# Optimization experiments

Measured on AMD Instinct MI355X. Metric: run time of the kernel, lower is better.

The kernel has to match this reference:

```python
import jax, jax.numpy as jnp
import numpy as np

N = 100000
E = 800000
D = 128
THETA = (0.5, 0.3, 0.2)
NEG_SLOPE = 0.01  # torch F.leaky_relu default


def setup_inputs() -> dict:
    key = jax.random.key(0)
    ks = jax.random.split(key, 16)
    inv = 1.0 / np.sqrt(D)
    return {
        "src": jax.random.randint(ks[0], (E,), 0, N),
        "dst": jax.random.randint(ks[1], (E,), 0, N),
        "x0": jax.random.normal(ks[2], (N, D), jnp.float32),
        "x": jax.random.normal(ks[3], (N, D), jnp.float32),
        "e": jax.random.normal(ks[4], (N, D), jnp.float32),
        "labels": jax.random.randint(ks[5], (N,), 0, 2),
        "nid": jax.random.randint(ks[6], (N // 2,), 0, N),
        "alpha": jnp.full((1,), 0.5, jnp.float32),
        "emb": jax.random.normal(ks[7], (3, D), jnp.float32).at[2].set(0.0),  # padding_idx=2
        "pred_w1": jax.random.normal(ks[8], (D, D), jnp.float32) * inv,
        "pred_b1": jnp.zeros((D,), jnp.float32),
        "pred_w2": jax.random.normal(ks[9], (2, D), jnp.float32) * inv,
        "pred_b2": jnp.zeros((2,), jnp.float32),
        "weights": jax.random.uniform(ks[10], (2 * D, D), jnp.float32, -inv, inv),
        "lin_w": jax.random.normal(ks[11], (D, 2 * D), jnp.float32) * inv,
        "lin_b": jnp.zeros((D,), jnp.float32),
    }


def reference(src, dst, x0, x, e, labels, nid, alpha, emb,
              pred_w1, pred_b1, pred_w2, pred_b2, weights, lin_w, lin_b):
    # Predictor: MLP -> 2 logits, prob of class 1
    h = jax.nn.relu(x @ pred_w1.T + pred_b1)
    logits = h @ pred_w2.T + pred_b2                     # [N, 2]
    prob = jax.nn.softmax(logits, axis=1)[:, 1]          # [N]

    # NodeLabelEmbedding: soft mix of rows 0 and 1
    x_node = (1.0 - prob)[:, None] * emb[0] + prob[:, None] * emb[1]
    x_ = x
    xk = x + alpha * x_node

    # degree norm from edge list (in-degrees at dst)
    degs = jax.ops.segment_sum(jnp.ones_like(dst, dtype=xk.dtype), dst, num_segments=N)
    dinv = jnp.clip(degs, 1.0, None) ** -0.5             # [N]
    dinv = dinv[:, None]

    def unn_laplacian(feat):
        # feat - D^-1/2 A D^-1/2 feat  (messages src -> dst)
        msg = jax.ops.segment_sum((feat * dinv)[src], dst, num_segments=N)
        return feat - msg * dinv

    hi = THETA[0] * xk
    for k in range(1, len(THETA)):
        xk = unn_laplacian(xk)
        hi = hi + THETA[k] * xk

    hi = jnp.concatenate([hi, x_], axis=1)               # [N, 2D]
    outputs = hi @ weights                               # [N, D]
    out = jnp.concatenate([e, outputs], axis=1)          # [N, 2D]
    out = jax.nn.leaky_relu(out @ lin_w.T + lin_b, NEG_SLOPE)
    return out + x0                                      # residual
```

## Files before the change

kernel.cpp:

```cpp
#include <hip/hip_runtime.h>

#define N_NODES 100000
#define N_EDGES 800000
#define D 128

#define G_MLP 1563
#define G_DEG 3125
#define G_PRE 192

typedef __attribute__((ext_vector_type(8))) short short8;
typedef __attribute__((ext_vector_type(4))) float f32x4;

__device__ inline unsigned short f2bf(float f) {
  unsigned u = __float_as_uint(f);
  unsigned r = (u + 0x7fffu + ((u >> 16) & 1u)) >> 16;
  return (unsigned short)r;
}
__device__ inline void bfma8(float* acc, const uint4 v, float d) {
  acc[0] = fmaf(__uint_as_float(v.x << 16), d, acc[0]);
  acc[1] = fmaf(__uint_as_float(v.x & 0xffff0000u), d, acc[1]);
  acc[2] = fmaf(__uint_as_float(v.y << 16), d, acc[2]);
  acc[3] = fmaf(__uint_as_float(v.y & 0xffff0000u), d, acc[3]);
  acc[4] = fmaf(__uint_as_float(v.z << 16), d, acc[4]);
  acc[5] = fmaf(__uint_as_float(v.z & 0xffff0000u), d, acc[5]);
  acc[6] = fmaf(__uint_as_float(v.w << 16), d, acc[6]);
  acc[7] = fmaf(__uint_as_float(v.w & 0xffff0000u), d, acc[7]);
}
__device__ inline void unpack8(float* o, const uint4 v) {
  o[0] = __uint_as_float(v.x << 16); o[1] = __uint_as_float(v.x & 0xffff0000u);
  o[2] = __uint_as_float(v.y << 16); o[3] = __uint_as_float(v.y & 0xffff0000u);
  o[4] = __uint_as_float(v.z << 16); o[5] = __uint_as_float(v.z & 0xffff0000u);
  o[6] = __uint_as_float(v.w << 16); o[7] = __uint_as_float(v.w & 0xffff0000u);
}
__device__ inline uint4 pack8(const float* v) {
  uint4 r;
  r.x = (unsigned)f2bf(v[0]) | ((unsigned)f2bf(v[1]) << 16);
  r.y = (unsigned)f2bf(v[2]) | ((unsigned)f2bf(v[3]) << 16);
  r.z = (unsigned)f2bf(v[4]) | ((unsigned)f2bf(v[5]) << 16);
  r.w = (unsigned)f2bf(v[6]) | ((unsigned)f2bf(v[7]) << 16);
  return r;
}

__global__ __launch_bounds__(256, 4)
void k_front(const float* __restrict__ x, const float* __restrict__ w1,
             const float* __restrict__ w2, const float* __restrict__ b1,
             const float* __restrict__ b2, const float* __restrict__ emb,
             const float* __restrict__ alpha_p, unsigned short* __restrict__ xk_bf,
             const int* __restrict__ dst, int* __restrict__ degs,
             const float* __restrict__ weights, const float* __restrict__ lin_w,
             unsigned short* __restrict__ wbt) {
  int tid = threadIdx.x;
  int bid = blockIdx.x;

  if (bid >= G_MLP) {
    if (bid < G_MLP + G_DEG) {
      int e = (bid - G_MLP) * 256 + tid;
      if (e < N_EDGES) atomicAdd(&degs[dst[e]], 1);
    } else {
      int gid = (bid - G_MLP - G_DEG) * 256 + tid;
      int k = gid >> 7, d = gid & 127;
      float v;
      if (k < 128) {
        v = lin_w[d * 256 + k];
      } else {
        const float* wrow = weights + (k - 128) * 128;
        const float* lcol = lin_w + d * 256 + 128;
        float s = 0.f;
        for (int j = 0; j < 128; j++) s += wrow[j] * lcol[j];
        v = s;
      }
      wbt[d * 392 + k] = f2bf(v);
    }
    return;
  }

  __shared__ __align__(16) float xsT[32 * 68];
  __shared__ __align__(16) float w1sT[32 * 128];
  __shared__ float zbuf[64];
  __shared__ float pbuf[64];

  int lane = tid & 63;
  int wave = tid >> 6;
  int n0 = bid * 64;

  int d8 = tid & 15;
  int n4 = tid >> 4;
  float acc[4][8];
  #pragma unroll
  for (int a = 0; a < 4; a++)
    #pragma unroll
    for (int c = 0; c < 8; c++) acc[a][c] = 0.f;

  for (int p = 0; p < 4; p++) {
    __syncthreads();
    {
      int j = tid >> 1;
      int kg0 = (tid & 1) * 4;
      const float4* wr = (const float4*)(w1 + j * 128 + p * 32);
      #pragma unroll
      for (int c = 0; c < 4; c++) {
        float4 v = wr[kg0 + c];
        int k = (kg0 + c) * 4;
        w1sT[(k + 0) * 128 + j] = v.x;
        w1sT[(k + 1) * 128 + j] = v.y;
        w1sT[(k + 2) * 128 + j] = v.z;
        w1sT[(k + 3) * 128 + j] = v.w;
      }
    }
    {
      int n = lane;
      int gn = n0 + n;
      int k8 = wave * 8;
      const float4* xr = (const float4*)(x + (size_t)gn * 128 + p * 32 + k8);
      float4 v0 = make_float4(0.f, 0.f, 0.f, 0.f), v1 = v0;
      if (gn < N_NODES) { v0 = xr[0]; v1 = xr[1]; }
      xsT[(k8 + 0) * 68 + n] = v0.x;
      xsT[(k8 + 1) * 68 + n] = v0.y;
      xsT[(k8 + 2) * 68 + n] = v0.z;
      xsT[(k8 + 3) * 68 + n] = v0.w;
      xsT[(k8 + 4) * 68 + n] = v1.x;
      xsT[(k8 + 5) * 68 + n] = v1.y;
      xsT[(k8 + 6) * 68 + n] = v1.z;
      xsT[(k8 + 7) * 68 + n] = v1.w;
    }
    __syncthreads();

    for (int kk = 0; kk < 32; kk += 4) {
      float wq[4][8];
      float4 f[4];
      #pragma unroll
      for (int q = 0; q < 4; q++) {
        const float4* wr = (const float4*)(w1sT + (kk + q) * 128 + d8 * 8);
        float4 a = wr[0], b = wr[1];
        wq[q][0] = a.x; wq[q][1] = a.y; wq[q][2] = a.z; wq[q][3] = a.w;
        wq[q][4] = b.x; wq[q][5] = b.y; wq[q][6] = b.z; wq[q][7] = b.w;
        f[q] = *(const float4*)(xsT + (kk + q) * 68 + n4 * 4);
      }
      #pragma unroll
      for (int q = 0; q < 4; q++) {
        #pragma unroll
        for (int c = 0; c < 8; c++) {
          acc[0][c] += f[q].x * wq[q][c];
          acc[1][c] += f[q].y * wq[q][c];
          acc[2][c] += f[q].z * wq[q][c];
          acc[3][c] += f[q].w * wq[q][c];
        }
      }
    }
  }

  {
    int j0 = d8 * 8;
    float bb[8], wd[8];
    #pragma unroll
    for (int c = 0; c < 8; c++) {
      bb[c] = b1[j0 + c];
      wd[c] = w2[128 + j0 + c] - w2[j0 + c];
    }
    #pragma unroll
    for (int a = 0; a < 4; a++) {
      float s = 0.f;
      #pragma unroll
      for (int c = 0; c < 8; c++) {
        float h = fmaxf(acc[a][c] + bb[c], 0.f);
        s += h * wd[c];
      }
      s += __shfl_down(s, 8);
      s += __shfl_down(s, 4);
      s += __shfl_down(s, 2);
      s += __shfl_down(s, 1);
      if (d8 == 0) zbuf[n4 * 4 + a] = s;
    }
  }
  __syncthreads();
  if (tid < 64) {
    float db2 = b2[1] - b2[0];
    float z = zbuf[tid] + db2;
    pbuf[tid] = 1.f / (1.f + expf(-z));
  }
  __syncthreads();

  {
    float al = alpha_p[0];
    int d4 = tid & 31;
    const float4 e0 = ((const float4*)emb)[d4];
    const float4 e1 = ((const float4*)(emb + 128))[d4];
    #pragma unroll
    for (int i = 0; i < 8; i++) {
      int n = i * 8 + (tid >> 5);
      int gn = n0 + n;
      if (gn >= N_NODES) continue;
      float p = pbuf[n];
      float c0 = al * (1.f - p), c1 = al * p;
      float4 xv = ((const float4*)x)[(size_t)gn * 32 + d4];
      float o0 = xv.x + c0 * e0.x + c1 * e1.x;
      float o1 = xv.y + c0 * e0.y + c1 * e1.y;
      float o2 = xv.z + c0 * e0.z + c1 * e1.z;
      float o3 = xv.w + c0 * e0.w + c1 * e1.w;
      ushort4 ov = make_ushort4(f2bf(o0), f2bf(o1), f2bf(o2), f2bf(o3));
      ((ushort4*)xk_bf)[(size_t)gn * 32 + d4] = ov;
    }
  }
}

__global__ void k_scan1(const int* __restrict__ degs, int* __restrict__ offs,
                        int* __restrict__ aux) {
  __shared__ int s[256];
  int tid = threadIdx.x;
  int i = blockIdx.x * 256 + tid;
  int v = (i < N_NODES) ? degs[i] : 0;
  int sum = v;
  s[tid] = sum; __syncthreads();
  for (int off = 1; off < 256; off <<= 1) {
    int t = (tid >= off) ? s[tid - off] : 0;
    __syncthreads();
    sum += t; s[tid] = sum;
    __syncthreads();
  }
  if (i < N_NODES) offs[i] = sum - v;
  if (tid == 255) aux[blockIdx.x] = sum;
}

__global__ void k_scan2(const int* __restrict__ aux, int* __restrict__ aux2, int nblk) {
  __shared__ int s[512];
  int tid = threadIdx.x;
  int v = (tid < nblk) ? aux[tid] : 0;
  int sum = v;
  s[tid] = sum; __syncthreads();
  for (int off = 1; off < 512; off <<= 1) {
    int t = (tid >= off) ? s[tid - off] : 0;
    __syncthreads();
    sum += t; s[tid] = sum;
    __syncthreads();
  }
  aux2[tid] = sum - v;
}

__global__ void k_scan3(int* __restrict__ offs, const int* __restrict__ aux2,
                        const int* __restrict__ degs, float* __restrict__ dinv) {
  int i = blockIdx.x * 256 + threadIdx.x;
  if (i < N_NODES) {
    offs[i] += aux2[blockIdx.x];
    dinv[i] = rsqrtf(fmaxf((float)degs[i], 1.0f));
  }
}

__global__ void k_fill(const int* __restrict__ src, const int* __restrict__ dst,
                       const int* __restrict__ offs, int* __restrict__ cursor,
                       int* __restrict__ csr) {
  int e = blockIdx.x * 256 + threadIdx.x;
  if (e < N_EDGES) {
    int d = dst[e];
    int pos = offs[d] + atomicAdd(&cursor[d], 1);
    csr[pos] = src[e];
  }
}

template <int PASS>
__global__ __launch_bounds__(256)
void k_gather(const unsigned short* __restrict__ feat,
              unsigned short* __restrict__ feat_out,
              float* __restrict__ hi,
              unsigned short* __restrict__ ahi,
              const int* __restrict__ csr, const int* __restrict__ offs,
              const int* __restrict__ degs, const float* __restrict__ dinv) {
  int node = blockIdx.x * 4 + (threadIdx.x >> 6);
  int lane = threadIdx.x & 63;
  int quad = lane >> 4;
  int l16 = lane & 15;
  int start = offs[node];
  int cnt = degs[node];
  const uint4* f16 = (const uint4*)feat;
  float acc[8];
  #pragma unroll
  for (int i = 0; i < 8; i++) acc[i] = 0.f;

  int j = 0;
  for (; j + 8 <= cnt; j += 8) {
    int sa = csr[start + j + quad];
    int sb = csr[start + j + 4 + quad];
    float da = dinv[sa], db = dinv[sb];
    uint4 va = f16[(size_t)sa * 16 + l16];
    uint4 vb = f16[(size_t)sb * 16 + l16];
    bfma8(acc, va, da);
    bfma8(acc, vb, db);
  }
  if (j + 4 <= cnt) {
    int s = csr[start + j + quad];
    float d = dinv[s];
    uint4 v = f16[(size_t)s * 16 + l16];
    bfma8(acc, v, d);
    j += 4;
  }
  int rem = cnt - j;
  if (quad < rem) {
    int s = csr[start + j + quad];
    float d = dinv[s];
    uint4 v = f16[(size_t)s * 16 + l16];
    bfma8(acc, v, d);
  }

  #pragma unroll
  for (int i = 0; i < 8; i++) {
    acc[i] += __shfl_down(acc[i], 32);
    acc[i] += __shfl_down(acc[i], 16);
  }

  if (quad == 0) {
    float dvi = dinv[node];
    float old[8], nw[8];
    unpack8(old, f16[(size_t)node * 16 + l16]);
    #pragma unroll
    for (int i = 0; i < 8; i++) nw[i] = old[i] - acc[i] * dvi;
    if (PASS == 1) {
      ((uint4*)feat_out)[(size_t)node * 16 + l16] = pack8(nw);
      float h[8];
      #pragma unroll
      for (int i = 0; i < 8; i++) h[i] = 0.5f * old[i] + 0.3f * nw[i];
      float4* hp = (float4*)(hi + (size_t)node * 128 + l16 * 8);
      hp[0] = make_float4(h[0], h[1], h[2], h[3]);
      hp[1] = make_float4(h[4], h[5], h[6], h[7]);
    } else {
      const float4* hp = (const float4*)(hi + (size_t)node * 128 + l16 * 8);
      float4 a = hp[0], b = hp[1];
      float h[8] = {a.x, a.y, a.z, a.w, b.x, b.y, b.z, b.w};
      #pragma unroll
      for (int i = 0; i < 8; i++) h[i] += 0.2f * nw[i];
      ((uint4*)ahi)[(size_t)node * 16 + l16] = pack8(h);
    }
  }
}

__global__ __launch_bounds__(256)
__attribute__((amdgpu_waves_per_eu(4, 4)))
void k_gemm2(const float* __restrict__ ein, const unsigned short* __restrict__ ahi,
             const float* __restrict__ x, const unsigned short* __restrict__ wbt,
             const float* __restrict__ lin_b, const float* __restrict__ x0,
             float* __restrict__ out) {
  __shared__ __align__(16) unsigned short Bs[32 * 392];
  int tid = threadIdx.x;
  int lane = tid & 63, wv = tid >> 6;
  int quad = lane >> 4, l16 = lane & 15;
  int n0 = blockIdx.x * 64;
  int rA = n0 + wv * 16 + l16;
  if (rA >= N_NODES) rA = N_NODES - 1;
  int kq = quad * 8;

  short8 af[12];
  #pragma unroll
  for (int kb = 0; kb < 4; kb++) {
    const float4* p = (const float4*)(ein + (size_t)rA * 128 + kb * 32 + kq);
    float4 a = p[0], b = p[1];
    short8 t;
    t[0] = (short)f2bf(a.x); t[1] = (short)f2bf(a.y);
    t[2] = (short)f2bf(a.z); t[3] = (short)f2bf(a.w);
    t[4] = (short)f2bf(b.x); t[5] = (short)f2bf(b.y);
    t[6] = (short)f2bf(b.z); t[7] = (short)f2bf(b.w);
    af[kb] = t;
  }
  #pragma unroll
  for (int kb = 0; kb < 4; kb++)
    af[4 + kb] = *(const short8*)(ahi + (size_t)rA * 128 + kb * 32 + kq);
  #pragma unroll
  for (int kb = 0; kb < 4; kb++) {
    const float4* p = (const float4*)(x + (size_t)rA * 128 + kb * 32 + kq);
    float4 a = p[0], b = p[1];
    short8 t;
    t[0] = (short)f2bf(a.x); t[1] = (short)f2bf(a.y);
    t[2] = (short)f2bf(a.z); t[3] = (short)f2bf(a.w);
    t[4] = (short)f2bf(b.x); t[5] = (short)f2bf(b.y);
    t[6] = (short)f2bf(b.z); t[7] = (short)f2bf(b.w);
    af[8 + kb] = t;
  }

  f32x4 acc[8];
  #pragma unroll
  for (int i = 0; i < 8; i++) acc[i] = (f32x4){0.f, 0.f, 0.f, 0.f};

  #pragma unroll
  for (int ch = 0; ch < 4; ch++) {
    if (ch) __syncthreads();
    {
      const uint4* W = (const uint4*)wbt;
      uint4* B4 = (uint4*)Bs;
      int r = tid >> 3, c0 = tid & 7;
      #pragma unroll
      for (int i = 0; i < 7; i++) {
        int c = c0 + i * 8;
        if (c < 49) B4[r * 49 + c] = W[(ch * 32 + r) * 49 + c];
      }
    }
    __syncthreads();
    #pragma unroll
    for (int kb = 0; kb < 12; kb++) {
      short8 a = af[kb];
      #pragma unroll
      for (int t = 0; t < 2; t++) {
        short8 b = *(const short8*)(Bs + (t * 16 + l16) * 392 + kb * 32 + kq);
        acc[ch * 2 + t] = __builtin_amdgcn_mfma_f32_16x16x32_bf16(a, b, acc[ch * 2 + t], 0, 0, 0);
      }
    }
  }

  #pragma unroll
  for (int idx = 0; idx < 8; idx++) {
    int col = (idx >> 1) * 32 + (idx & 1) * 16 + l16;
    float bl = lin_b[col];
    #pragma unroll
    for (int r = 0; r < 4; r++) {
      int gn = n0 + wv * 16 + quad * 4 + r;
      if (gn < N_NODES) {
        float v = acc[idx][r] + bl;
        v = (v > 0.f) ? v : 0.01f * v;
        out[(size_t)gn * 128 + col] = v + x0[(size_t)gn * 128 + col];
      }
    }
  }
}

extern "C" void kernel_launch(void* const* d_in, const int* in_sizes, int n_in,
                              void* d_out, int out_size, void* d_ws, size_t ws_size,
                              hipStream_t stream) {
  const int*   src     = (const int*)d_in[0];
  const int*   dst     = (const int*)d_in[1];
  const float* x0      = (const float*)d_in[2];
  const float* x       = (const float*)d_in[3];
  const float* ein     = (const float*)d_in[4];
  const float* alpha   = (const float*)d_in[7];
  const float* emb     = (const float*)d_in[8];
  const float* w1      = (const float*)d_in[9];
  const float* b1      = (const float*)d_in[10];
  const float* w2      = (const float*)d_in[11];
  const float* b2      = (const float*)d_in[12];
  const float* weights = (const float*)d_in[13];
  const float* lin_w   = (const float*)d_in[14];
  const float* lin_b   = (const float*)d_in[15];
  float* out = (float*)d_out;

  unsigned short* xk_bf  = (unsigned short*)d_ws;
  unsigned short* xk1_bf = xk_bf  + (size_t)N_NODES * 128;
  unsigned short* ahi    = xk1_bf + (size_t)N_NODES * 128;
  unsigned short* wbt    = ahi    + (size_t)N_NODES * 128;
  float* dinv = (float*)(wbt + 128 * 392);
  int* degs   = (int*)(dinv + N_NODES);
  int* offs   = degs + N_NODES;
  int* cursor = offs + N_NODES;
  int* aux    = cursor + N_NODES;
  int* aux2   = aux + 512;
  int* csr    = aux2 + 512;

  hipMemsetAsync(degs, 0, sizeof(int) * 3 * (size_t)N_NODES, stream);

  int gN = (N_NODES + 255) / 256;
  int gE = (N_EDGES + 255) / 256;

  k_front<<<G_MLP + G_DEG + G_PRE, 256, 0, stream>>>(
      x, w1, w2, b1, b2, emb, alpha, xk_bf, dst, degs, weights, lin_w, wbt);

  k_scan1<<<gN, 256, 0, stream>>>(degs, offs, aux);
  k_scan2<<<1, 512, 0, stream>>>(aux, aux2, gN);
  k_scan3<<<gN, 256, 0, stream>>>(offs, aux2, degs, dinv);
  k_fill <<<gE, 256, 0, stream>>>(src, dst, offs, cursor, csr);

  float* hi = out;
  k_gather<1><<<N_NODES / 4, 256, 0, stream>>>(xk_bf,  xk1_bf, hi, nullptr, csr, offs, degs, dinv);
  k_gather<2><<<N_NODES / 4, 256, 0, stream>>>(xk1_bf, nullptr, hi, ahi,    csr, offs, degs, dinv);

  k_gemm2<<<(N_NODES + 63) / 64, 256, 0, stream>>>(ein, ahi, x, wbt, lin_b, x0, out);
}
```

Baseline: 449.5 us.

## Read GEMM2 weight fragments directly from global memory instead of LDS staging

The final GEMM kernel no longer stages the combined weight matrix into shared memory in four chunks with barriers. Each lane now loads its B fragments straight from global (cache-resident) weights, and A fragments are converted per k-step inside the loop rather than all held in registers up front. This removes LDS traffic, barriers and the occupancy cap, trading them for many more global/L1 loads of the small weight matrix per wave.

```diff
diff --git a/kernel.cpp b/kernel.cpp
--- a/kernel.cpp
+++ b/kernel.cpp
@@ -332,12 +332,10 @@
 }
 
 __global__ __launch_bounds__(256)
-__attribute__((amdgpu_waves_per_eu(4, 4)))
 void k_gemm2(const float* __restrict__ ein, const unsigned short* __restrict__ ahi,
              const float* __restrict__ x, const unsigned short* __restrict__ wbt,
              const float* __restrict__ lin_b, const float* __restrict__ x0,
              float* __restrict__ out) {
-  __shared__ __align__(16) unsigned short Bs[32 * 392];
   int tid = threadIdx.x;
   int lane = tid & 63, wv = tid >> 6;
   int quad = lane >> 4, l16 = lane & 15;
@@ -346,71 +344,48 @@
   if (rA >= N_NODES) rA = N_NODES - 1;
   int kq = quad * 8;
 
-  short8 af[12];
-  #pragma unroll
-  for (int kb = 0; kb < 4; kb++) {
-    const float4* p = (const float4*)(ein + (size_t)rA * 128 + kb * 32 + kq);
-    float4 a = p[0], b = p[1];
-    short8 t;
-    t[0] = (short)f2bf(a.x); t[1] = (short)f2bf(a.y);
-    t[2] = (short)f2bf(a.z); t[3] = (short)f2bf(a.w);
-    t[4] = (short)f2bf(b.x); t[5] = (short)f2bf(b.y);
-    t[6] = (short)f2bf(b.z); t[7] = (short)f2bf(b.w);
-    af[kb] = t;
-  }
-  #pragma unroll
-  for (int kb = 0; kb < 4; kb++)
-    af[4 + kb] = *(const short8*)(ahi + (size_t)rA * 128 + kb * 32 + kq);
-  #pragma unroll
-  for (int kb = 0; kb < 4; kb++) {
-    const float4* p = (const float4*)(x + (size_t)rA * 128 + kb * 32 + kq);
-    float4 a = p[0], b = p[1];
-    short8 t;
-    t[0] = (short)f2bf(a.x); t[1] = (short)f2bf(a.y);
-    t[2] = (short)f2bf(a.z); t[3] = (short)f2bf(a.w);
-    t[4] = (short)f2bf(b.x); t[5] = (short)f2bf(b.y);
-    t[6] = (short)f2bf(b.z); t[7] = (short)f2bf(b.w);
-    af[8 + kb] = t;
-  }
-
   f32x4 acc[8];
   #pragma unroll
   for (int i = 0; i < 8; i++) acc[i] = (f32x4){0.f, 0.f, 0.f, 0.f};
 
-  #pragma unroll
-  for (int ch = 0; ch < 4; ch++) {
-    if (ch) __syncthreads();
-    {
-      const uint4* W = (const uint4*)wbt;
-      uint4* B4 = (uint4*)Bs;
-      int r = tid >> 3, c0 = tid & 7;
-      #pragma unroll
-      for (int i = 0; i < 7; i++) {
-        int c = c0 + i * 8;
-        if (c < 49) B4[r * 49 + c] = W[(ch * 32 + r) * 49 + c];
-      }
-    }
-    __syncthreads();
-    #pragma unroll
-    for (int kb = 0; kb < 12; kb++) {
-      short8 a = af[kb];
-      #pragma unroll
-      for (int t = 0; t < 2; t++) {
-        short8 b = *(const short8*)(Bs + (t * 16 + l16) * 392 + kb * 32 + kq);
-        acc[ch * 2 + t] = __builtin_amdgcn_mfma_f32_16x16x32_bf16(a, b, acc[ch * 2 + t], 0, 0, 0);
-      }
-    }
-  }
-
-  #pragma unroll
-  for (int idx = 0; idx < 8; idx++) {
-    int col = (idx >> 1) * 32 + (idx & 1) * 16 + l16;
+  const unsigned short* bp = wbt + (size_t)l16 * 392 + kq;
+
+  #pragma unroll
+  for (int kb = 0; kb < 12; kb++) {
+    short8 a;
+    if (kb < 4) {
+      const float4* p = (const float4*)(ein + (size_t)rA * 128 + kb * 32 + kq);
+      float4 u = p[0], v = p[1];
+      a[0] = (short)f2bf(u.x); a[1] = (short)f2bf(u.y);
+      a[2] = (short)f2bf(u.z); a[3] = (short)f2bf(u.w);
+      a[4] = (short)f2bf(v.x); a[5] = (short)f2bf(v.y);
+      a[6] = (short)f2bf(v.z); a[7] = (short)f2bf(v.w);
+    } else if (kb < 8) {
+      a = *(const short8*)(ahi + (size_t)rA * 128 + (kb - 4) * 32 + kq);
+    } else {
+      const float4* p = (const float4*)(x + (size_t)rA * 128 + (kb - 8) * 32 + kq);
+      float4 u = p[0], v = p[1];
+      a[0] = (short)f2bf(u.x); a[1] = (short)f2bf(u.y);
+      a[2] = (short)f2bf(u.z); a[3] = (short)f2bf(u.w);
+      a[4] = (short)f2bf(v.x); a[5] = (short)f2bf(v.y);
+      a[6] = (short)f2bf(v.z); a[7] = (short)f2bf(v.w);
+    }
+    #pragma unroll
+    for (int ct = 0; ct < 8; ct++) {
+      short8 b = *(const short8*)(bp + (size_t)ct * 16 * 392 + kb * 32);
+      acc[ct] = __builtin_amdgcn_mfma_f32_16x16x32_bf16(a, b, acc[ct], 0, 0, 0);
+    }
+  }
+
+  #pragma unroll
+  for (int ct = 0; ct < 8; ct++) {
+    int col = ct * 16 + l16;
     float bl = lin_b[col];
     #pragma unroll
     for (int r = 0; r < 4; r++) {
       int gn = n0 + wv * 16 + quad * 4 + r;
       if (gn < N_NODES) {
-        float v = acc[idx][r] + bl;
+        float v = acc[ct][r] + bl;
         v = (v > 0.f) ? v : 0.01f * v;
         out[(size_t)gn * 128 + col] = v + x0[(size_t)gn * 128 + col];
       }
```

Result: slower. 490.4 us (+9.1%).

## Pre-swizzle GEMM weights into MFMA fragment order and double-buffer LDS loads

Applied to the files above, without the earlier changes.

The weight-prep stage now stores the combined bf16 weight matrix already laid out in the MFMA B-fragment order, so each lane reads one contiguous 16-byte vector from LDS. The final GEMM kernel double-buffers the weight chunks, prefetching the next chunk into registers while the MFMAs for the current chunk run, which removes one barrier per chunk. The fixed waves-per-EU attribute is also dropped. LDS use grows to two 24 KB buffers, which may lower occupancy.

```diff
diff --git a/kernel.cpp b/kernel.cpp
--- a/kernel.cpp
+++ b/kernel.cpp
@@ -48,7 +48,7 @@
              const float* __restrict__ alpha_p, unsigned short* __restrict__ xk_bf,
              const int* __restrict__ dst, int* __restrict__ degs,
              const float* __restrict__ weights, const float* __restrict__ lin_w,
-             unsigned short* __restrict__ wbt) {
+             unsigned short* __restrict__ wfr) {
   int tid = threadIdx.x;
   int bid = blockIdx.x;
 
@@ -69,7 +69,10 @@
         for (int j = 0; j < 128; j++) s += wrow[j] * lcol[j];
         v = s;
       }
-      wbt[d * 392 + k] = f2bf(v);
+      int ct = d >> 4, kb = k >> 5;
+      int lane = (((k >> 3) & 3) << 4) | (d & 15);
+      int j = k & 7;
+      wfr[((ct * 12 + kb) << 9) + (lane << 3) + j] = f2bf(v);
     }
     return;
   }
@@ -332,12 +335,11 @@
 }
 
 __global__ __launch_bounds__(256)
-__attribute__((amdgpu_waves_per_eu(4, 4)))
 void k_gemm2(const float* __restrict__ ein, const unsigned short* __restrict__ ahi,
-             const float* __restrict__ x, const unsigned short* __restrict__ wbt,
+             const float* __restrict__ x, const unsigned short* __restrict__ wfr,
              const float* __restrict__ lin_b, const float* __restrict__ x0,
              float* __restrict__ out) {
-  __shared__ __align__(16) unsigned short Bs[32 * 392];
+  __shared__ __align__(16) unsigned short Bs[2][24 * 512];
   int tid = threadIdx.x;
   int lane = tid & 63, wv = tid >> 6;
   int quad = lane >> 4, l16 = lane & 15;
@@ -377,40 +379,53 @@
   #pragma unroll
   for (int i = 0; i < 8; i++) acc[i] = (f32x4){0.f, 0.f, 0.f, 0.f};
 
+  const uint4* W4 = (const uint4*)wfr;
+
+  {
+    uint4 tmp[6];
+    #pragma unroll
+    for (int i = 0; i < 6; i++) tmp[i] = W4[tid + i * 256];
+    uint4* B4 = (uint4*)Bs[0];
+    #pragma unroll
+    for (int i = 0; i < 6; i++) B4[tid + i * 256] = tmp[i];
+  }
+  __syncthreads();
+
   #pragma unroll
   for (int ch = 0; ch < 4; ch++) {
-    if (ch) __syncthreads();
-    {
-      const uint4* W = (const uint4*)wbt;
-      uint4* B4 = (uint4*)Bs;
-      int r = tid >> 3, c0 = tid & 7;
-      #pragma unroll
-      for (int i = 0; i < 7; i++) {
-        int c = c0 + i * 8;
-        if (c < 49) B4[r * 49 + c] = W[(ch * 32 + r) * 49 + c];
-      }
-    }
-    __syncthreads();
-    #pragma unroll
-    for (int kb = 0; kb < 12; kb++) {
-      short8 a = af[kb];
-      #pragma unroll
-      for (int t = 0; t < 2; t++) {
-        short8 b = *(const short8*)(Bs + (t * 16 + l16) * 392 + kb * 32 + kq);
-        acc[ch * 2 + t] = __builtin_amdgcn_mfma_f32_16x16x32_bf16(a, b, acc[ch * 2 + t], 0, 0, 0);
-      }
-    }
-  }
-
-  #pragma unroll
-  for (int idx = 0; idx < 8; idx++) {
-    int col = (idx >> 1) * 32 + (idx & 1) * 16 + l16;
+    int cur = ch & 1;
+    uint4 tmp[6];
+    if (ch < 3) {
+      #pragma unroll
+      for (int i = 0; i < 6; i++) tmp[i] = W4[(ch + 1) * 1536 + tid + i * 256];
+    }
+    const unsigned short* Bc = Bs[cur];
+    #pragma unroll
+    for (int ctl = 0; ctl < 2; ctl++) {
+      #pragma unroll
+      for (int kb = 0; kb < 12; kb++) {
+        short8 b = *(const short8*)(Bc + (ctl * 12 + kb) * 512 + (lane << 3));
+        acc[ch * 2 + ctl] =
+            __builtin_amdgcn_mfma_f32_16x16x32_bf16(af[kb], b, acc[ch * 2 + ctl], 0, 0, 0);
+      }
+    }
+    if (ch < 3) {
+      uint4* B4 = (uint4*)Bs[cur ^ 1];
+      #pragma unroll
+      for (int i = 0; i < 6; i++) B4[tid + i * 256] = tmp[i];
+      __syncthreads();
+    }
+  }
+
+  #pragma unroll
+  for (int ct = 0; ct < 8; ct++) {
+    int col = ct * 16 + l16;
     float bl = lin_b[col];
     #pragma unroll
     for (int r = 0; r < 4; r++) {
       int gn = n0 + wv * 16 + quad * 4 + r;
       if (gn < N_NODES) {
-        float v = acc[idx][r] + bl;
+        float v = acc[ct][r] + bl;
         v = (v > 0.f) ? v : 0.01f * v;
         out[(size_t)gn * 128 + col] = v + x0[(size_t)gn * 128 + col];
       }
@@ -440,8 +455,8 @@
   unsigned short* xk_bf  = (unsigned short*)d_ws;
   unsigned short* xk1_bf = xk_bf  + (size_t)N_NODES * 128;
   unsigned short* ahi    = xk1_bf + (size_t)N_NODES * 128;
-  unsigned short* wbt    = ahi    + (size_t)N_NODES * 128;
-  float* dinv = (float*)(wbt + 128 * 392);
+  unsigned short* wfr    = ahi    + (size_t)N_NODES * 128;
+  float* dinv = (float*)(wfr + 128 * 392);
   int* degs   = (int*)(dinv + N_NODES);
   int* offs   = degs + N_NODES;
   int* cursor = offs + N_NODES;
@@ -455,7 +470,7 @@
   int gE = (N_EDGES + 255) / 256;
 
   k_front<<<G_MLP + G_DEG + G_PRE, 256, 0, stream>>>(
-      x, w1, w2, b1, b2, emb, alpha, xk_bf, dst, degs, weights, lin_w, wbt);
+      x, w1, w2, b1, b2, emb, alpha, xk_bf, dst, degs, weights, lin_w, wfr);
 
   k_scan1<<<gN, 256, 0, stream>>>(degs, offs, aux);
   k_scan2<<<1, 512, 0, stream>>>(aux, aux2, gN);
@@ -466,5 +481,5 @@
   k_gather<1><<<N_NODES / 4, 256, 0, stream>>>(xk_bf,  xk1_bf, hi, nullptr, csr, offs, degs, dinv);
   k_gather<2><<<N_NODES / 4, 256, 0, stream>>>(xk1_bf, nullptr, hi, ahi,    csr, offs, degs, dinv);
 
-  k_gemm2<<<(N_NODES + 63) / 64, 256, 0, stream>>>(ein, ahi, x, wbt, lin_b, x0, out);
-}
+  k_gemm2<<<(N_NODES + 63) / 64, 256, 0, stream>>>(ein, ahi, x, wfr, lin_b, x0, out);
+}
```

Result: no change. 445.3 us (-0.9%).
